# Kernel optimization log

Hardware: AMD Instinct MI355X
Metric: run time of the kernel (lower is better)

## Reference

```python
import jax, jax.numpy as jnp
import numpy as np

MAX_OBJECTS = 65536
K = 8            # slots_per_object
D = 256          # d_memory
M = 65536        # number of objects stored this frame (unique indices)


def setup_inputs() -> dict:
    key = jax.random.key(0)
    k1, k2, k3, k4, k5 = jax.random.split(key, 5)
    return {
        "memory": jax.random.normal(k1, (MAX_OBJECTS, K, D), dtype=jnp.float32),
        "capture_poses": jax.random.normal(k2, (MAX_OBJECTS, K, 4, 4), dtype=jnp.float32),
        "slot_filled": jnp.zeros((MAX_OBJECTS, K), dtype=bool),
        "slot_count": jax.random.randint(k3, (MAX_OBJECTS,), 0, 9, dtype=jnp.int32),
        "object_indices": jnp.arange(M, dtype=jnp.int32),
        "features": jax.random.normal(k4, (M, D), dtype=jnp.float32),
        "camera_pose": jax.random.normal(k5, (4, 4), dtype=jnp.float32),
    }


def _pose_deltas(camera_pose, stored_poses):
    # camera_pose: (4,4); stored_poses: (M,K,4,4) -> deltas (M,K)
    R_curr = camera_pose[:3, :3]               # (3,3)
    t_curr = camera_pose[:3, 3]                # (3,)
    R_s = stored_poses[:, :, :3, :3]           # (M,K,3,3)
    t_s = stored_poses[:, :, :3, 3]            # (M,K,3)
    # R_curr @ R_s^T per (m,k): [i,l] = sum_j R_curr[i,j] * R_s[m,k,l,j]
    R_diff = jnp.einsum('ij,mklj->mkil', R_curr, R_s)
    eye = jnp.eye(3, dtype=R_diff.dtype)
    rot_delta = jnp.linalg.norm((R_diff - eye).reshape(*R_diff.shape[:2], 9), axis=-1)
    trans_delta = jnp.linalg.norm(t_curr - t_s, axis=-1)
    return rot_delta + trans_delta             # (M,K)


def reference(memory, capture_poses, slot_filled, slot_count, object_indices, features, camera_pose):
    """Vectorized equivalent of store(): per object, fill next slot if not full,
    else evict the slot with the most similar capture pose. Indices are unique,
    so all M updates are independent and match the sequential torch loop."""
    k = memory.shape[1]
    cnt = slot_count[object_indices]                      # (M,)
    stored = capture_poses[object_indices]                # (M,K,4,4)
    deltas = _pose_deltas(camera_pose, stored)            # (M,K)
    evict_slot = jnp.argmin(deltas, axis=-1).astype(cnt.dtype)
    fill_branch = cnt < k                                 # (M,) bool
    slot = jnp.where(fill_branch, cnt, evict_slot)        # (M,)

    mem_new = memory.at[object_indices, slot].set(features)
    poses_new = capture_poses.at[object_indices, slot].set(camera_pose)
    filled_new = slot_filled.at[object_indices, slot].set(True)
    count_new = slot_count.at[object_indices].add(fill_branch.astype(slot_count.dtype))
    return mem_new, poses_new, filled_new, count_new
```

## Files before the change

kernel.cpp:

```cpp
#include <hip/hip_runtime.h>

#define MAXOBJ 65536
#define KSLOTS 8
#define DFEAT 256


__global__ void init_slots_kernel(int* __restrict__ slots, int n) {
    int i = blockIdx.x * blockDim.x + threadIdx.x;
    if (i < n) slots[i] = -1;
}

__global__ void slot_compute_kernel(const float* __restrict__ capture_poses,
                                    const int* __restrict__ slot_count,
                                    const int* __restrict__ object_indices,
                                    const float* __restrict__ camera_pose,
                                    int* __restrict__ slots,
                                    int* __restrict__ srcs,
                                    int M) {
    int m = blockIdx.x * blockDim.x + threadIdx.x;
    if (m >= M) return;
    int obj = object_indices[m];

    float Rc[3][3], tc[3];
#pragma unroll
    for (int i = 0; i < 3; i++) {
        Rc[i][0] = camera_pose[i * 4 + 0];
        Rc[i][1] = camera_pose[i * 4 + 1];
        Rc[i][2] = camera_pose[i * 4 + 2];
        tc[i]    = camera_pose[i * 4 + 3];
    }

    int cnt = slot_count[obj];
    const float* ps = capture_poses + (size_t)obj * (KSLOTS * 16);

    float best = 3.4e38f;
    int bestk = 0;
#pragma unroll
    for (int k = 0; k < KSLOTS; k++) {
        const float* p = ps + k * 16;
        float rot = 0.f;
#pragma unroll
        for (int i = 0; i < 3; i++) {
#pragma unroll
            for (int l = 0; l < 3; l++) {
                float v = Rc[i][0] * p[l * 4 + 0] + Rc[i][1] * p[l * 4 + 1] + Rc[i][2] * p[l * 4 + 2];
                v -= (i == l) ? 1.f : 0.f;
                rot += v * v;
            }
        }
        float tx = tc[0] - p[3];
        float ty = tc[1] - p[7];
        float tz = tc[2] - p[11];
        float delta = sqrtf(rot) + sqrtf(tx * tx + ty * ty + tz * tz);
        if (delta < best) { best = delta; bestk = k; }
    }

    int fill = (cnt < KSLOTS) ? 1 : 0;
    int slot = fill ? cnt : bestk;
    slots[obj] = slot;
    srcs[obj] = m;
}

__global__ void small_outputs_kernel(const unsigned char* __restrict__ slot_filled,
                                     const int* __restrict__ slot_count,
                                     const int* __restrict__ slots,
                                     float* __restrict__ filled_out,
                                     float* __restrict__ count_out) {
    int obj = blockIdx.x * blockDim.x + threadIdx.x;
    if (obj >= MAXOBJ) return;
    int slot = slots[obj];
    int cnt = slot_count[obj];
    int fill = (slot >= 0 && cnt < KSLOTS) ? 1 : 0;
    count_out[obj] = (float)(cnt + fill);
#pragma unroll
    for (int k = 0; k < KSLOTS; k++) {
        int was = slot_filled[obj * KSLOTS + k] != 0;
        filled_out[obj * KSLOTS + k] = (was || k == slot) ? 1.0f : 0.0f;
    }
}

__global__ void mem_copy_kernel(const float4* __restrict__ memory,
                                const float4* __restrict__ features,
                                const int* __restrict__ slots,
                                const int* __restrict__ srcs,
                                float4* __restrict__ out) {
    int i = blockIdx.x * blockDim.x + threadIdx.x;
    if (i >= MAXOBJ * KSLOTS * (DFEAT / 4)) return;
    int elem = i * 4;
    int obj = elem >> 11;
    int k   = (elem >> 8) & 7;
    int d4  = i & (DFEAT / 4 - 1);
    int slot = slots[obj];
    float4 v;
    if (k == slot) {
        v = features[(size_t)srcs[obj] * (DFEAT / 4) + d4];
    } else {
        v = memory[i];
    }
    out[i] = v;
}

__global__ void pose_copy_kernel(const float4* __restrict__ capture_poses,
                                 const float4* __restrict__ camera_pose,
                                 const int* __restrict__ slots,
                                 float4* __restrict__ out) {
    int i = blockIdx.x * blockDim.x + threadIdx.x;
    if (i >= MAXOBJ * KSLOTS * 4) return;
    int elem = i * 4;
    int obj = elem >> 7;
    int k   = (elem >> 4) & 7;
    int r4  = i & 3;
    int slot = slots[obj];
    float4 v = (k == slot) ? camera_pose[r4] : capture_poses[i];
    out[i] = v;
}

extern "C" void kernel_launch(void* const* d_in, const int* in_sizes, int n_in,
                              void* d_out, int out_size, void* d_ws, size_t ws_size,
                              hipStream_t stream) {
    const float*         memory        = (const float*)d_in[0];
    const float*         capture_poses = (const float*)d_in[1];
    const unsigned char* slot_filled   = (const unsigned char*)d_in[2];
    const int*           slot_count    = (const int*)d_in[3];
    const int*           object_indices= (const int*)d_in[4];
    const float*         features      = (const float*)d_in[5];
    const float*         camera_pose   = (const float*)d_in[6];
    const int M = in_sizes[4];

    float* out = (float*)d_out;
    float* mem_out    = out;
    float* poses_out  = out + (size_t)MAXOBJ * KSLOTS * DFEAT;
    float* filled_out = poses_out + (size_t)MAXOBJ * KSLOTS * 16;
    float* count_out  = filled_out + (size_t)MAXOBJ * KSLOTS;

    int* slots = (int*)d_ws;
    int* srcs  = slots + MAXOBJ;

    const int B = 256;

    init_slots_kernel<<<(MAXOBJ + B - 1) / B, B, 0, stream>>>(slots, MAXOBJ);

    slot_compute_kernel<<<(M + B - 1) / B, B, 0, stream>>>(
        capture_poses, slot_count, object_indices, camera_pose, slots, srcs, M);

    small_outputs_kernel<<<(MAXOBJ + B - 1) / B, B, 0, stream>>>(
        slot_filled, slot_count, slots, filled_out, count_out);

    const int mem4 = MAXOBJ * KSLOTS * (DFEAT / 4);
    mem_copy_kernel<<<(mem4 + B - 1) / B, B, 0, stream>>>(
        (const float4*)memory, (const float4*)features, slots, srcs, (float4*)mem_out);

    const int pose4 = MAXOBJ * KSLOTS * 4;
    pose_copy_kernel<<<(pose4 + B - 1) / B, B, 0, stream>>>(
        (const float4*)capture_poses, (const float4*)camera_pose, slots, (float4*)poses_out);
}
```

Before: 219.2 us.

## Fuse memory, pose, filled and count copies into one per-object kernel

Replaces three separate output kernels with one kernel launched one block per object, which copies the 8x256 memory rows, the 8 poses, the filled flags and the count. Slot and source indices are read once per block instead of once per element. The bulk memory copy uses nontemporal loads and stores to avoid polluting cache with streaming data. This saves two launches and the redundant per-thread index lookups, at the cost of idle threads in the small-output sections.

```diff
diff --git a/kernel.cpp b/kernel.cpp
--- a/kernel.cpp
+++ b/kernel.cpp
@@ -3,6 +3,8 @@
 #define MAXOBJ 65536
 #define KSLOTS 8
 #define DFEAT 256
+
+typedef float f32x4 __attribute__((ext_vector_type(4)));
 
 
 __global__ void init_slots_kernel(int* __restrict__ slots, int n) {
@@ -61,58 +63,66 @@
     srcs[obj] = m;
 }
 
-__global__ void small_outputs_kernel(const unsigned char* __restrict__ slot_filled,
-                                     const int* __restrict__ slot_count,
-                                     const int* __restrict__ slots,
-                                     float* __restrict__ filled_out,
-                                     float* __restrict__ count_out) {
-    int obj = blockIdx.x * blockDim.x + threadIdx.x;
-    if (obj >= MAXOBJ) return;
-    int slot = slots[obj];
-    int cnt = slot_count[obj];
-    int fill = (slot >= 0 && cnt < KSLOTS) ? 1 : 0;
-    count_out[obj] = (float)(cnt + fill);
-#pragma unroll
-    for (int k = 0; k < KSLOTS; k++) {
+__global__ void fused_copy_kernel(const f32x4* __restrict__ memory,
+                                  const f32x4* __restrict__ features,
+                                  const f32x4* __restrict__ capture_poses,
+                                  const f32x4* __restrict__ camera_pose,
+                                  const unsigned char* __restrict__ slot_filled,
+                                  const int* __restrict__ slot_count,
+                                  const int* __restrict__ slots,
+                                  const int* __restrict__ srcs,
+                                  f32x4* __restrict__ mem_out,
+                                  f32x4* __restrict__ poses_out,
+                                  float* __restrict__ filled_out,
+                                  float* __restrict__ count_out) {
+    const int obj = blockIdx.x;
+    const int t = threadIdx.x;
+    const int slot = slots[obj];
+    const int src  = srcs[obj];
+
+    const size_t base = (size_t)obj * (KSLOTS * DFEAT / 4);
+    const int d4 = t & 63;
+
+    {
+        const int k = t >> 6;
+        f32x4 v;
+        if (k == slot) {
+            v = features[(size_t)src * (DFEAT / 4) + d4];
+        } else {
+            v = __builtin_nontemporal_load(&memory[base + t]);
+        }
+        __builtin_nontemporal_store(v, &mem_out[base + t]);
+    }
+    {
+        const int k = 4 + (t >> 6);
+        f32x4 v;
+        if (k == slot) {
+            v = features[(size_t)src * (DFEAT / 4) + d4];
+        } else {
+            v = __builtin_nontemporal_load(&memory[base + 256 + t]);
+        }
+        __builtin_nontemporal_store(v, &mem_out[base + 256 + t]);
+    }
+
+    if (t < 32) {
+        const int k  = t >> 2;
+        const int r4 = t & 3;
+        const size_t pbase = (size_t)obj * (KSLOTS * 16 / 4);
+        f32x4 v = (k == slot) ? camera_pose[r4] : capture_poses[pbase + t];
+        poses_out[pbase + t] = v;
+    }
+
+    if (t >= 64 && t < 64 + KSLOTS) {
+        const int k = t - 64;
         int was = slot_filled[obj * KSLOTS + k] != 0;
         filled_out[obj * KSLOTS + k] = (was || k == slot) ? 1.0f : 0.0f;
     }
-}
 
-__global__ void mem_copy_kernel(const float4* __restrict__ memory,
-                                const float4* __restrict__ features,
-                                const int* __restrict__ slots,
-                                const int* __restrict__ srcs,
-                                float4* __restrict__ out) {
-    int i = blockIdx.x * blockDim.x + threadIdx.x;
-    if (i >= MAXOBJ * KSLOTS * (DFEAT / 4)) return;
-    int elem = i * 4;
-    int obj = elem >> 11;
-    int k   = (elem >> 8) & 7;
-    int d4  = i & (DFEAT / 4 - 1);
-    int slot = slots[obj];
-    float4 v;
-    if (k == slot) {
-        v = features[(size_t)srcs[obj] * (DFEAT / 4) + d4];
-    } else {
-        v = memory[i];
+    if (t == 96) {
+        int cnt = slot_count[obj];
+        int fill = (slot >= 0 && cnt < KSLOTS) ? 1 : 0;
+        count_out[obj] = (float)(cnt + fill);
     }
-    out[i] = v;
-}
-
-__global__ void pose_copy_kernel(const float4* __restrict__ capture_poses,
-                                 const float4* __restrict__ camera_pose,
-                                 const int* __restrict__ slots,
-                                 float4* __restrict__ out) {
-    int i = blockIdx.x * blockDim.x + threadIdx.x;
-    if (i >= MAXOBJ * KSLOTS * 4) return;
-    int elem = i * 4;
-    int obj = elem >> 7;
-    int k   = (elem >> 4) & 7;
-    int r4  = i & 3;
-    int slot = slots[obj];
-    float4 v = (k == slot) ? camera_pose[r4] : capture_poses[i];
-    out[i] = v;
 }
 
 extern "C" void kernel_launch(void* const* d_in, const int* in_sizes, int n_in,
@@ -143,14 +153,9 @@
     slot_compute_kernel<<<(M + B - 1) / B, B, 0, stream>>>(
         capture_poses, slot_count, object_indices, camera_pose, slots, srcs, M);
 
-    small_outputs_kernel<<<(MAXOBJ + B - 1) / B, B, 0, stream>>>(
-        slot_filled, slot_count, slots, filled_out, count_out);
-
-    const int mem4 = MAXOBJ * KSLOTS * (DFEAT / 4);
-    mem_copy_kernel<<<(mem4 + B - 1) / B, B, 0, stream>>>(
-        (const float4*)memory, (const float4*)features, slots, srcs, (float4*)mem_out);
-
-    const int pose4 = MAXOBJ * KSLOTS * 4;
-    pose_copy_kernel<<<(pose4 + B - 1) / B, B, 0, stream>>>(
-        (const float4*)capture_poses, (const float4*)camera_pose, slots, (float4*)poses_out);
+    fused_copy_kernel<<<MAXOBJ, B, 0, stream>>>(
+        (const f32x4*)memory, (const f32x4*)features,
+        (const f32x4*)capture_poses, (const f32x4*)camera_pose,
+        slot_filled, slot_count, slots, srcs,
+        (f32x4*)mem_out, (f32x4*)poses_out, filled_out, count_out);
 }
```

Measured after the change: 209.9 us. -4.2%, faster.
